# Kernel tuning notes

Hardware: AMD Instinct MI355X
Metric: run time of the kernel (lower is better)

The kernel has to match this reference:

```python
import jax, jax.numpy as jnp
import numpy as np

EPS = 1e-12
IMU_NOISE_DIAG = np.array([1e-07, 1e-07, 0.01, 0.001], dtype=np.float32)
INIT_COVAR_SQRT = np.array([0, 0, 0, 0, 0, 0, 0.01, 0.01, 0.01, 1e-4, 1e-4, 1e-4,
                            1e-08, 1e-08, 1e-08, 0.1, 0.1, 0.1], dtype=np.float32)
TRANS_SCALE = 5.4
TS2 = TRANS_SCALE * TRANS_SCALE
VIS_INIT_GUESS = 10.0 / TS2
VIS_BETA, VIS_GAMMA = 3.0, 1.0
IMU_BETA, IMU_GAMMA = 4.0, 1.0


def skew3(v):  # (..., 3) -> (..., 3, 3)
    x, y, z = v[..., 0], v[..., 1], v[..., 2]
    o = jnp.zeros_like(x)
    return jnp.stack([jnp.stack([o, -z, y], -1),
                      jnp.stack([z, o, -x], -1),
                      jnp.stack([-y, x, o], -1)], -2)


def exp_SO3(phi):  # (..., 3) -> (..., 3, 3) Rodrigues
    theta2 = jnp.sum(phi * phi, axis=-1)
    theta = jnp.sqrt(theta2)
    small = theta < 1e-8
    th = jnp.where(small, 1.0, theta)
    A = jnp.where(small, 1.0 - theta2 / 6.0, jnp.sin(th) / th)[..., None, None]
    B = jnp.where(small, 0.5 - theta2 / 24.0, (1.0 - jnp.cos(th)) / (th * th))[..., None, None]
    K = skew3(phi)
    return jnp.eye(3, dtype=phi.dtype) + A * K + B * (K @ K)


def force_symmetrical(M):
    Mu = jnp.triu(M)
    n = M.shape[-1]
    return Mu + jnp.swapaxes(Mu, -1, -2) * (1.0 - jnp.eye(n, dtype=M.dtype))


def proc_vis_covar(vis_std):
    # vis_covar_scale is all ones (par.vis_covar_scale = 1.0)
    scale = jnp.ones((6,), dtype=vis_std.dtype)
    diag = VIS_INIT_GUESS * (10.0 ** (VIS_BETA * jnp.tanh(VIS_GAMMA * vis_std)))
    diag = diag / scale[None, :]
    return jax.vmap(jnp.diag)(diag)  # (2B, 6, 6)


def get_imu_noise_covar(imu_noise_weight):
    # Linear(1,4,bias=False) applied to ones(1): just the weight column
    covar = 10.0 ** (IMU_BETA * jnp.tanh(IMU_GAMMA * imu_noise_weight[:, 0]))  # (4,)
    diag = jnp.repeat(jnp.asarray(IMU_NOISE_DIAG), 3) * jnp.repeat(covar, 3)   # (12,)
    return jnp.diag(diag)


def propagate(dts, wa_xyzs, R_ckbts, g_k, imu_noise_covar, P0):
    B = dts.shape[0]
    T = dts.shape[1]
    I3 = jnp.eye(3, dtype=dts.dtype)
    I18 = jnp.eye(18, dtype=dts.dtype)

    def step(P, inp):
        dt, gyro, accel, R = inp  # (B,), (B,3), (B,3), (B,3,3)
        Rt = jnp.swapaxes(R, -1, -2)
        w = gyro  # bw_k = 0
        Rg = jnp.einsum('bij,bj->bi', Rt, g_k)
        a = accel - Rg  # ba_k = 0
        F = jnp.zeros((B, 18, 18), dtype=dt.dtype)
        F = F.at[:, 0:3, 0:3].set(-skew3(w))
        F = F.at[:, 0:3, 12:15].set(-I3)
        F = F.at[:, 3:6, 6:9].set(I3)
        F = F.at[:, 6:9, 0:3].set(-jnp.einsum('bij,bjk->bik', R, skew3(Rg + a)))
        F = F.at[:, 6:9, 9:12].set(-I3)
        F = F.at[:, 6:9, 15:18].set(-R)
        G = jnp.zeros((B, 18, 12), dtype=dt.dtype)
        G = G.at[:, 0:3, 0:3].set(-I3)
        G = G.at[:, 6:9, 6:9].set(-R)
        G = G.at[:, 12:15, 3:6].set(I3)
        G = G.at[:, 15:18, 9:12].set(I3)
        dtb = dt[:, None, None]
        Phi = I18 + F * dtb + 0.5 * (F @ F) * (dtb * dtb)
        Phi = Phi.at[:, 0:3, 0:3].set(jnp.swapaxes(exp_SO3(dt[:, None] * w), -1, -2))
        PhiT = jnp.swapaxes(Phi, -1, -2)
        Q = (Phi @ G @ imu_noise_covar @ jnp.swapaxes(G, -1, -2) @ PhiT) * dtb
        P = force_symmetrical(Phi @ P @ PhiT + Q)
        return P, None

    xs = (jnp.swapaxes(dts, 0, 1),                       # (T, B)
          jnp.swapaxes(wa_xyzs[:, :T, :3], 0, 1),        # (T, B, 3)
          jnp.swapaxes(wa_xyzs[:, :T, 3:], 0, 1),        # (T, B, 3)
          jnp.swapaxes(R_ckbts[:, :T], 0, 1))            # (T, B, 3, 3)
    P, _ = jax.lax.scan(step, P0, xs)
    return P


def update(preimu_rot, preimu_trans, P, vis_rot, vis_trans, vis_covar, H0, H1, v_ck, g_ck):
    B = vis_rot.shape[0]
    residual = jnp.concatenate([vis_rot - preimu_rot, vis_trans - preimu_trans], axis=1)  # (B,6)
    I3 = jnp.eye(3, dtype=vis_rot.dtype)
    H = jnp.zeros((B, 6, 18), dtype=vis_rot.dtype)
    H = H.at[:, 0:3, 0:3].set(H0)
    H = H.at[:, 3:6, 0:3].set(H1)
    H = H.at[:, 3:6, 3:6].set(I3)
    Ht = jnp.swapaxes(H, -1, -2)
    S = H @ P @ Ht + vis_covar                 # (B,6,6)
    K = P @ Ht @ jnp.linalg.inv(S)             # (B,18,6)
    est = K @ residual[..., None]              # (B,18,1)
    phi_e, p_e = est[:, 0:3], est[:, 3:6]
    v_e, g_e = est[:, 6:9], est[:, 9:12]
    ekf_phi = preimu_rot + (H0 @ phi_e)[..., 0]
    ekf_t = preimu_trans + (H1 @ phi_e)[..., 0] + p_e[..., 0]
    return ekf_phi, ekf_t, v_ck + v_e[..., 0], g_ck + g_e[..., 0]


def setup_inputs() -> dict:
    key = jax.random.key(0)
    ks = jax.random.split(key, 16)
    B2 = 8192
    d = {
        'dts': jax.random.uniform(ks[0], (B2, 11), jnp.float32) * 0.01,
        'wa_xyzs': jax.random.normal(ks[1], (B2, 12, 6), jnp.float32),
        'R_ckbts': jax.random.normal(ks[2], (B2, 12, 3, 3), jnp.float32),
        'velocities': jax.random.normal(ks[3], (B2, 3), jnp.float32),
        'gravities': jax.random.normal(ks[4], (B2, 3), jnp.float32),
        'H0': jax.random.normal(ks[5], (B2, 3, 3), jnp.float32),
        'H1': jax.random.normal(ks[6], (B2, 3, 3), jnp.float32),
        'preimu_rot': jax.random.normal(ks[7], (B2, 3), jnp.float32),
        'preimu_trans': jax.random.normal(ks[8], (B2, 3), jnp.float32),
        'vis_rot': jax.random.normal(ks[9], (B2, 3), jnp.float32),
        'vis_trans': jax.random.normal(ks[10], (B2, 3), jnp.float32),
        'vis_rot_std': jax.random.uniform(ks[11], (B2, 3), jnp.float32),
        'vis_trans_std': jax.random.uniform(ks[12], (B2, 3), jnp.float32),
        'init_covar_diag_sqrt': jnp.asarray(INIT_COVAR_SQRT),
        'imu_noise_weight': jnp.zeros((4, 1), jnp.float32),  # train_imu_noise_covar=False -> zeroed
    }
    return d


def reference(dts, wa_xyzs, R_ckbts, velocities, gravities, H0, H1,
              preimu_rot, preimu_trans, vis_rot, vis_trans,
              vis_rot_std, vis_trans_std, init_covar_diag_sqrt, imu_noise_weight):
    B2 = dts.shape[0]
    vis_std = jnp.concatenate([vis_rot_std, vis_trans_std], axis=1)
    vis_covar = proc_vis_covar(vis_std)
    vis_trans = vis_trans * TRANS_SCALE
    imu_noise_covar = get_imu_noise_covar(imu_noise_weight)
    P0_diag = init_covar_diag_sqrt * init_covar_diag_sqrt + EPS
    P0 = jnp.broadcast_to(jnp.diag(P0_diag), (B2, 18, 18))
    P = propagate(dts, wa_xyzs, R_ckbts, gravities, imu_noise_covar, P0)
    ekf_phi, ekf_t, ekf_v, ekf_g = update(preimu_rot, preimu_trans, P,
                                          vis_rot, vis_trans, vis_covar,
                                          H0, H1, velocities, gravities)
    return jnp.concatenate([ekf_phi, ekf_t, ekf_v, ekf_g], axis=1)  # (2B, 12)
```

## Files before the change

### kernel.cpp

```cpp
#include <hip/hip_runtime.h>
#include <math.h>

#define TSTEPS 11
#define PPB 7
#define LPP 9
#define IN_STRIDE 196
#define WSTRIDE 228
#define PHT_OFF 0
#define S6_OFF 144
#define Y_OFF 192
#define EST_OFF 200

__device__ __forceinline__ float sel3(int c, float a, float b, float d) {
    float t = (c == 1) ? b : a;
    return (c == 2) ? d : t;
}

__device__ __forceinline__ size_t umin_sz(size_t a, size_t b) { return a < b ? a : b; }

__global__ void __launch_bounds__(64)
ekf_kernel(const float* __restrict__ dts, const float* __restrict__ wa,
           const float* __restrict__ Rc, const float* __restrict__ vel,
           const float* __restrict__ grav, const float* __restrict__ H0g,
           const float* __restrict__ H1g, const float* __restrict__ prot,
           const float* __restrict__ ptrans, const float* __restrict__ vrot,
           const float* __restrict__ vtrans, const float* __restrict__ vrstd,
           const float* __restrict__ vtstd, const float* __restrict__ icds,
           const float* __restrict__ inw, float* __restrict__ out, int B)
{
    __shared__ __align__(16) float gin[PPB * IN_STRIDE];
    __shared__ __align__(16) float lds[PPB * WSTRIDE];
    const int tid = threadIdx.x;
    const int praw = tid / LPP;
    const int r = tid - praw * LPP;
    const int p = (praw < PPB) ? praw : (PPB - 1);
    const int blk0 = blockIdx.x * PPB;
    const int b0 = blk0 + p;
    const bool valid = (praw < PPB) && (b0 < B);
    const int b = (b0 < B) ? b0 : (B - 1);
    float* L = lds + p * WSTRIDE;
    const float* gi = gin + p * IN_STRIDE;

    {
        const size_t dmax = (size_t)B * 11 - 1;
        for (int e = tid; e < PPB * 11; e += 64) {
            const int pp = e / 11, o = e - pp * 11;
            gin[pp * IN_STRIDE + o] = dts[umin_sz((size_t)blk0 * 11 + e, dmax)];
        }
        const size_t wmax4 = (size_t)B * 18 - 1;
        const float4* wa4 = (const float4*)wa;
        for (int e = tid; e < PPB * 18; e += 64) {
            const int pp = e / 18, o = e - pp * 18;
            *(float4*)&gin[pp * IN_STRIDE + 12 + o * 4] = wa4[umin_sz((size_t)blk0 * 18 + e, wmax4)];
        }
        const size_t rmax4 = (size_t)B * 27 - 1;
        const float4* Rc4 = (const float4*)Rc;
        for (int e = tid; e < PPB * 27; e += 64) {
            const int pp = e / 27, o = e - pp * 27;
            *(float4*)&gin[pp * IN_STRIDE + 84 + o * 4] = Rc4[umin_sz((size_t)blk0 * 27 + e, rmax4)];
        }
    }

    float h0v[9], h1v[9];
#pragma unroll
    for (int i = 0; i < 9; ++i) { h0v[i] = H0g[(size_t)b * 9 + i]; h1v[i] = H1g[(size_t)b * 9 + i]; }
    const int rc6 = (r < 6) ? r : 5;
    const float* hpr = (rc6 < 3) ? (H0g + (size_t)b * 9 + rc6 * 3)
                                 : (H1g + (size_t)b * 9 + (rc6 - 3) * 3);
    const float hr0 = hpr[0], hr1 = hpr[1], hr2 = hpr[2];
    const float sdv = (rc6 < 3) ? vrstd[(size_t)b * 3 + rc6] : vtstd[(size_t)b * 3 + (rc6 - 3)];
    const float rsa = (rc6 < 3) ? vrot[(size_t)b * 3 + rc6] : vtrans[(size_t)b * 3 + (rc6 - 3)];
    const float rsb = (rc6 < 3) ? prot[(size_t)b * 3 + rc6] : ptrans[(size_t)b * 3 + (rc6 - 3)];
    const float velv = vel[(size_t)b * 3 + ((r >= 6) ? (r - 6) : 0)];

    const float qcA = 1e-7f * exp10f(4.f * tanhf(inw[0]));
    const float qcB = 1e-7f * exp10f(4.f * tanhf(inw[1]));
    const float qcC = 1e-2f * exp10f(4.f * tanhf(inw[2]));
    const float qcD = 1e-3f * exp10f(4.f * tanhf(inw[3]));

    const float g0 = grav[(size_t)b*3+0], g1 = grav[(size_t)b*3+1], g2 = grav[(size_t)b*3+2];

    float np[18], npb[18];
#pragma unroll
    for (int k = 0; k < 18; ++k) { np[k] = 0.f; npb[k] = 0.f; }
    { const float d0 = icds[r];     np[r]      = d0*d0 + 1e-12f;
      const float d1 = icds[9 + r]; npb[9 + r] = d1*d1 + 1e-12f; }

    __syncthreads();

    for (int t = 0; t < TSTEPS; ++t) {
        const float dt = gi[t];
        const float2 wq0 = *(const float2*)&gi[12 + t * 6];
        const float2 wq1 = *(const float2*)&gi[12 + t * 6 + 2];
        const float2 wq2 = *(const float2*)&gi[12 + t * 6 + 4];
        const float w0 = wq0.x, w1 = wq0.y, w2 = wq1.x;
        const float ar0 = wq1.y, ar1 = wq2.x, ar2 = wq2.y;
        float Rm[9];
#pragma unroll
        for (int i = 0; i < 9; ++i) Rm[i] = gi[84 + t * 9 + i];

        const float hdt2 = 0.5f * dt * dt;
        const float Rg0 = Rm[0]*g0 + Rm[3]*g1 + Rm[6]*g2;
        const float Rg1 = Rm[1]*g0 + Rm[4]*g1 + Rm[7]*g2;
        const float Rg2 = Rm[2]*g0 + Rm[5]*g1 + Rm[8]*g2;
        const float a0 = Rg0 + (ar0 - Rg0);
        const float a1 = Rg1 + (ar1 - Rg1);
        const float a2 = Rg2 + (ar2 - Rg2);

        const float p0 = dt*w0, p1 = dt*w1, p2 = dt*w2;
        const float th2 = p0*p0 + p1*p1 + p2*p2;
        const float th4 = th2 * th2;
        const float A  = 1.f - th2*(1.f/6.f)  + th4*(1.f/120.f);
        const float Bc = 0.5f - th2*(1.f/24.f) + th4*(1.f/720.f);
        float E[9];
        E[0] =  Bc*(p0*p0 - th2);  E[1] =  A*p2 + Bc*p0*p1;  E[2] = -A*p1 + Bc*p0*p2;
        E[3] = -A*p2 + Bc*p1*p0;   E[4] =  Bc*(p1*p1 - th2); E[5] =  A*p0 + Bc*p1*p2;
        E[6] =  A*p1 + Bc*p2*p0;   E[7] = -A*p0 + Bc*p2*p1;  E[8] =  Bc*(p2*p2 - th2);
        float N[9];
        N[0] = -(Rm[1]*a2 - Rm[2]*a1);  N[1] = -(Rm[2]*a0 - Rm[0]*a2);  N[2] = -(Rm[0]*a1 - Rm[1]*a0);
        N[3] = -(Rm[4]*a2 - Rm[5]*a1);  N[4] = -(Rm[5]*a0 - Rm[3]*a2);  N[5] = -(Rm[3]*a1 - Rm[4]*a0);
        N[6] = -(Rm[7]*a2 - Rm[8]*a1);  N[7] = -(Rm[8]*a0 - Rm[6]*a2);  N[8] = -(Rm[6]*a1 - Rm[7]*a0);
        float M2[9];
#pragma unroll
        for (int c = 0; c < 3; ++c) {
            const float n0 = N[c*3], n1 = N[c*3+1], n2 = N[c*3+2];
            M2[c*3+0] = dt*n0 - hdt2*(n1*w2 - n2*w1);
            M2[c*3+1] = dt*n1 - hdt2*(n2*w0 - n0*w2);
            M2[c*3+2] = dt*n2 - hdt2*(n0*w1 - n1*w0);
        }

        auto Smv = [&](const float v[18], float o[9]) {
            const float ev0 = E[0]*v[0] + E[1]*v[1] + E[2]*v[2];
            const float ev1 = E[3]*v[0] + E[4]*v[1] + E[5]*v[2];
            const float ev2 = E[6]*v[0] + E[7]*v[1] + E[8]*v[2];
            const float cx0 = w1*v[14] - w2*v[13];
            const float cx1 = w2*v[12] - w0*v[14];
            const float cx2 = w0*v[13] - w1*v[12];
            o[0] = ev0 - dt*v[12] + hdt2*cx0;
            o[1] = ev1 - dt*v[13] + hdt2*cx1;
            o[2] = ev2 - dt*v[14] + hdt2*cx2;
            const float nv0 = N[0]*v[0] + N[1]*v[1] + N[2]*v[2];
            const float nv1 = N[3]*v[0] + N[4]*v[1] + N[5]*v[2];
            const float nv2 = N[6]*v[0] + N[7]*v[1] + N[8]*v[2];
            const float rv0 = Rm[0]*v[15] + Rm[1]*v[16] + Rm[2]*v[17];
            const float rv1 = Rm[3]*v[15] + Rm[4]*v[16] + Rm[5]*v[17];
            const float rv2 = Rm[6]*v[15] + Rm[7]*v[16] + Rm[8]*v[17];
            o[3] = hdt2*nv0 + dt*v[6] - hdt2*v[9]  - hdt2*rv0;
            o[4] = hdt2*nv1 + dt*v[7] - hdt2*v[10] - hdt2*rv1;
            o[5] = hdt2*nv2 + dt*v[8] - hdt2*v[11] - hdt2*rv2;
            const float mv0 = M2[0]*v[0] + M2[1]*v[1] + M2[2]*v[2];
            const float mv1 = M2[3]*v[0] + M2[4]*v[1] + M2[5]*v[2];
            const float mv2 = M2[6]*v[0] + M2[7]*v[1] + M2[8]*v[2];
            const float nw0 = N[0]*v[12] + N[1]*v[13] + N[2]*v[14];
            const float nw1 = N[3]*v[12] + N[4]*v[13] + N[5]*v[14];
            const float nw2 = N[6]*v[12] + N[7]*v[13] + N[8]*v[14];
            o[6] = mv0 - dt*v[9]  - hdt2*nw0 - dt*rv0;
            o[7] = mv1 - dt*v[10] - hdt2*nw1 - dt*rv1;
            o[8] = mv2 - dt*v[11] - hdt2*nw2 - dt*rv2;
        };

        float uca[9], ucb[9];
        Smv(np, uca);
        Smv(npb, ucb);
#pragma unroll
        for (int i = 0; i < 9; ++i) {
            L[i*20 + r]     = uca[i];
            L[i*20 + 9 + r] = ucb[i];
        }
        __syncthreads();

        float ur[18];
        {
            const float4* up = (const float4*)&L[r*20];
            const float4 q0 = up[0], q1 = up[1], q2 = up[2], q3 = up[3];
            const float2 q4 = *(const float2*)&L[r*20 + 16];
            ur[0]=q0.x; ur[1]=q0.y; ur[2]=q0.z; ur[3]=q0.w;
            ur[4]=q1.x; ur[5]=q1.y; ur[6]=q1.z; ur[7]=q1.w;
            ur[8]=q2.x; ur[9]=q2.y; ur[10]=q2.z; ur[11]=q2.w;
            ur[12]=q3.x; ur[13]=q3.y; ur[14]=q3.z; ur[15]=q3.w;
            ur[16]=q4.x; ur[17]=q4.y;
        }

        float w9[9];
        Smv(ur, w9);

        const int c6 = (r >= 6) ? (r - 6) : 0;
        const float rc0 = sel3(c6, Rm[0], Rm[3], Rm[6]);
        const float rc1 = sel3(c6, Rm[1], Rm[4], Rm[7]);
        const float rc2 = sel3(c6, Rm[2], Rm[5], Rm[8]);
        const float dq = dt * qcC;
        const float q0v = dq * (Rm[0]*rc0 + Rm[1]*rc1 + Rm[2]*rc2);
        const float q1v = dq * (Rm[3]*rc0 + Rm[4]*rc1 + Rm[5]*rc2);
        const float q2v = dq * (Rm[6]*rc0 + Rm[7]*rc1 + Rm[8]*rc2);

#pragma unroll
        for (int i = 0; i < 9; ++i)
            np[i] = np[i] + uca[i] + ur[i] + w9[i];
        if (r < 3) np[r] += dt * qcA;
        if (r >= 6) { np[6] += q0v; np[7] += q1v; np[8] += q2v; }
#pragma unroll
        for (int i = 9; i < 18; ++i) np[i] += ur[i];

#pragma unroll
        for (int i = 0; i < 9; ++i) npb[i] += ucb[i];
        if (r >= 3) npb[9 + r] += dt * ((r < 6) ? qcB : qcD);

        __syncthreads();
    }

    float phtA[6], phtB[6];
#pragma unroll
    for (int m = 0; m < 3; ++m) {
        phtA[m] = np[0]*h0v[m*3] + np[1]*h0v[m*3+1] + np[2]*h0v[m*3+2];
        phtB[m] = npb[0]*h0v[m*3] + npb[1]*h0v[m*3+1] + npb[2]*h0v[m*3+2];
    }
#pragma unroll
    for (int m = 3; m < 6; ++m) {
        phtA[m] = np[0]*h1v[(m-3)*3] + np[1]*h1v[(m-3)*3+1] + np[2]*h1v[(m-3)*3+2] + np[m];
        phtB[m] = npb[0]*h1v[(m-3)*3] + npb[1]*h1v[(m-3)*3+1] + npb[2]*h1v[(m-3)*3+2] + npb[m];
    }
#pragma unroll
    for (int m = 0; m < 6; ++m) {
        L[PHT_OFF + r*8 + m]       = phtA[m];
        L[PHT_OFF + (9 + r)*8 + m] = phtB[m];
    }
    __syncthreads();

    if (valid && r < 6) {
        const float VIG = (float)(10.0 / (5.4 * 5.4));
#pragma unroll
        for (int n = 0; n < 6; ++n) {
            float v = hr0 * L[PHT_OFF + 0*8 + n] + hr1 * L[PHT_OFF + 1*8 + n]
                    + hr2 * L[PHT_OFF + 2*8 + n];
            if (r >= 3) v += phtA[n];
            if (n == r) v += VIG * exp10f(3.f * tanhf(sdv));
            L[S6_OFF + r*8 + n] = v;
        }
        L[S6_OFF + r*8 + 6] = (r < 3) ? (rsa - rsb) : (rsa * 5.4f - rsb);
    }
    __syncthreads();

    if (valid && r == 0) {
        float a[6][7];
        const float* Sb = &L[S6_OFF];
#pragma unroll
        for (int m = 0; m < 6; ++m) {
            const float4 q0 = *(const float4*)&Sb[m*8];
            const float4 q1 = *(const float4*)&Sb[m*8 + 4];
            a[m][0]=q0.x; a[m][1]=q0.y; a[m][2]=q0.z; a[m][3]=q0.w;
            a[m][4]=q1.x; a[m][5]=q1.y; a[m][6]=q1.z;
        }
#pragma unroll
        for (int k = 0; k < 6; ++k) {
#pragma unroll
            for (int j = k + 1; j < 6; ++j) {
                const bool c = fabsf(a[j][k]) > fabsf(a[k][k]);
#pragma unroll
                for (int cc = k; cc < 7; ++cc) {
                    const float hi = c ? a[j][cc] : a[k][cc];
                    const float lo = c ? a[k][cc] : a[j][cc];
                    a[k][cc] = hi; a[j][cc] = lo;
                }
            }
            const float inv = 1.f / a[k][k];
#pragma unroll
            for (int j = 0; j < 6; ++j) {
                if (j == k) continue;
                const float f = a[j][k] * inv;
#pragma unroll
                for (int cc = k + 1; cc < 7; ++cc) a[j][cc] -= f * a[k][cc];
            }
        }
#pragma unroll
        for (int m = 0; m < 6; ++m) L[Y_OFF + m] = a[m][6] / a[m][m];
    }
    __syncthreads();

    float ym[6];
#pragma unroll
    for (int m = 0; m < 6; ++m) ym[m] = L[Y_OFF + m];
    float estr = 0.f, est9 = 0.f;
#pragma unroll
    for (int m = 0; m < 6; ++m) { estr += phtA[m]*ym[m]; est9 += phtB[m]*ym[m]; }
    if (valid) {
        L[EST_OFF + r] = estr;
        if (r < 3) L[EST_OFF + 9 + r] = est9;
    }
    __syncthreads();

    const float e0 = L[EST_OFF + 0], e1 = L[EST_OFF + 1], e2 = L[EST_OFF + 2];
    if (valid) {
        float o;
        if (r < 3) {
            o = rsb + hr0*e0 + hr1*e1 + hr2*e2;
        } else if (r < 6) {
            o = rsb + hr0*e0 + hr1*e1 + hr2*e2 + estr;
        } else {
            o = velv + estr;
        }
        out[(size_t)b*12 + r] = o;
        if (r < 3) out[(size_t)b*12 + 9 + r] = ((r==0)?g0:((r==1)?g1:g2)) + est9;
    }
}

extern "C" void kernel_launch(void* const* d_in, const int* in_sizes, int n_in,
                              void* d_out, int out_size, void* d_ws, size_t ws_size,
                              hipStream_t stream) {
    const float* dts    = (const float*)d_in[0];
    const float* wa     = (const float*)d_in[1];
    const float* Rc     = (const float*)d_in[2];
    const float* vel    = (const float*)d_in[3];
    const float* grav   = (const float*)d_in[4];
    const float* H0g    = (const float*)d_in[5];
    const float* H1g    = (const float*)d_in[6];
    const float* prot   = (const float*)d_in[7];
    const float* ptrans = (const float*)d_in[8];
    const float* vrot   = (const float*)d_in[9];
    const float* vtrans = (const float*)d_in[10];
    const float* vrstd  = (const float*)d_in[11];
    const float* vtstd  = (const float*)d_in[12];
    const float* icds   = (const float*)d_in[13];
    const float* inw    = (const float*)d_in[14];
    float* outp = (float*)d_out;

    const int B = in_sizes[0] / TSTEPS;
    const int grid = (B + PPB - 1) / PPB;
    hipLaunchKernelGGL(ekf_kernel, dim3(grid), dim3(64), 0, stream,
                       dts, wa, Rc, vel, grav, H0g, H1g, prot, ptrans,
                       vrot, vtrans, vrstd, vtstd, icds, inw, outp, B);
}
```

Measured before the change: 33.73 us.

## Exploit sparse bottom-right covariance block and prefetch next step inputs

Each lane now holds only the lower-right diagonal entry and the off-diagonal cross terms of the covariance block. The bottom-block matrix-vector product is replaced by a closed-form sparse update that uses per-lane column selects of R, N and the gyro skew matrix. Shared-memory input is repacked into a per-timestep record with a stride of 20, and the next step's inputs are read during the current step so LDS latency overlaps compute. The change relies on the bottom-right block staying diagonal, and it adds select logic plus scalar rather than vector global loads during staging.

```diff
diff --git a/kernel.cpp b/kernel.cpp
--- a/kernel.cpp
+++ b/kernel.cpp
@@ -4,7 +4,7 @@
 #define TSTEPS 11
 #define PPB 7
 #define LPP 9
-#define IN_STRIDE 196
+#define IN_STRIDE 228
 #define WSTRIDE 228
 #define PHT_OFF 0
 #define S6_OFF 144
@@ -45,19 +45,21 @@
         const size_t dmax = (size_t)B * 11 - 1;
         for (int e = tid; e < PPB * 11; e += 64) {
             const int pp = e / 11, o = e - pp * 11;
-            gin[pp * IN_STRIDE + o] = dts[umin_sz((size_t)blk0 * 11 + e, dmax)];
-        }
-        const size_t wmax4 = (size_t)B * 18 - 1;
-        const float4* wa4 = (const float4*)wa;
-        for (int e = tid; e < PPB * 18; e += 64) {
-            const int pp = e / 18, o = e - pp * 18;
-            *(float4*)&gin[pp * IN_STRIDE + 12 + o * 4] = wa4[umin_sz((size_t)blk0 * 18 + e, wmax4)];
-        }
-        const size_t rmax4 = (size_t)B * 27 - 1;
-        const float4* Rc4 = (const float4*)Rc;
-        for (int e = tid; e < PPB * 27; e += 64) {
-            const int pp = e / 27, o = e - pp * 27;
-            *(float4*)&gin[pp * IN_STRIDE + 84 + o * 4] = Rc4[umin_sz((size_t)blk0 * 27 + e, rmax4)];
+            gin[pp * IN_STRIDE + o * 20] = dts[umin_sz((size_t)blk0 * 11 + e, dmax)];
+        }
+        const size_t wmax = (size_t)B * 72 - 1;
+        for (int e = tid; e < PPB * 66; e += 64) {
+            const int pp = e / 66, o = e - pp * 66;
+            const int t = o / 6, k = o - t * 6;
+            gin[pp * IN_STRIDE + t * 20 + 2 + k] =
+                wa[umin_sz((size_t)blk0 * 72 + (size_t)pp * 72 + o, wmax)];
+        }
+        const size_t rmax = (size_t)B * 108 - 1;
+        for (int e = tid; e < PPB * 99; e += 64) {
+            const int pp = e / 99, o = e - pp * 99;
+            const int t = o / 9, k = o - t * 9;
+            gin[pp * IN_STRIDE + t * 20 + 8 + k] =
+                Rc[umin_sz((size_t)blk0 * 108 + (size_t)pp * 108 + o, rmax)];
         }
     }
 
@@ -80,24 +82,43 @@
 
     const float g0 = grav[(size_t)b*3+0], g1 = grav[(size_t)b*3+1], g2 = grav[(size_t)b*3+2];
 
-    float np[18], npb[18];
-#pragma unroll
-    for (int k = 0; k < 18; ++k) { np[k] = 0.f; npb[k] = 0.f; }
-    { const float d0 = icds[r];     np[r]      = d0*d0 + 1e-12f;
-      const float d1 = icds[9 + r]; npb[9 + r] = d1*d1 + 1e-12f; }
-
-    __syncthreads();
+    float np[18], ncr[9];
+#pragma unroll
+    for (int k = 0; k < 18; ++k) np[k] = 0.f;
+#pragma unroll
+    for (int k = 0; k < 9; ++k) ncr[k] = 0.f;
+    float d_br;
+    { const float d0 = icds[r];     np[r] = d0*d0 + 1e-12f;
+      const float d1 = icds[9 + r]; d_br  = d1*d1 + 1e-12f; }
+
+    const int cls = (r < 3) ? 0 : ((r < 6) ? 1 : 2);
+    const int c3 = r - 3 * cls;
+
+    __syncthreads();
+
+    float dt = gi[0];
+    float w0, w1, w2, ar0, ar1, ar2, Rm[9];
+    {
+        const float2 qa = *(const float2*)&gi[2];
+        const float2 qb = *(const float2*)&gi[4];
+        const float2 qc = *(const float2*)&gi[6];
+        w0 = qa.x; w1 = qa.y; w2 = qb.x; ar0 = qb.y; ar1 = qc.x; ar2 = qc.y;
+        const float4 r0 = *(const float4*)&gi[8];
+        const float4 r1 = *(const float4*)&gi[12];
+        Rm[0]=r0.x; Rm[1]=r0.y; Rm[2]=r0.z; Rm[3]=r0.w;
+        Rm[4]=r1.x; Rm[5]=r1.y; Rm[6]=r1.z; Rm[7]=r1.w;
+        Rm[8]=gi[16];
+    }
 
     for (int t = 0; t < TSTEPS; ++t) {
-        const float dt = gi[t];
-        const float2 wq0 = *(const float2*)&gi[12 + t * 6];
-        const float2 wq1 = *(const float2*)&gi[12 + t * 6 + 2];
-        const float2 wq2 = *(const float2*)&gi[12 + t * 6 + 4];
-        const float w0 = wq0.x, w1 = wq0.y, w2 = wq1.x;
-        const float ar0 = wq1.y, ar1 = wq2.x, ar2 = wq2.y;
-        float Rm[9];
-#pragma unroll
-        for (int i = 0; i < 9; ++i) Rm[i] = gi[84 + t * 9 + i];
+        const int tn = (t + 1 < TSTEPS) ? (t + 1) : t;
+        const float dt_n = gi[tn*20];
+        const float2 nqa = *(const float2*)&gi[tn*20 + 2];
+        const float2 nqb = *(const float2*)&gi[tn*20 + 4];
+        const float2 nqc = *(const float2*)&gi[tn*20 + 6];
+        const float4 nr0 = *(const float4*)&gi[tn*20 + 8];
+        const float4 nr1 = *(const float4*)&gi[tn*20 + 12];
+        const float nr8 = gi[tn*20 + 16];
 
         const float hdt2 = 0.5f * dt * dt;
         const float Rg0 = Rm[0]*g0 + Rm[3]*g1 + Rm[6]*g2;
@@ -159,9 +180,46 @@
             o[8] = mv2 - dt*v[11] - hdt2*nw2 - dt*rv2;
         };
 
-        float uca[9], ucb[9];
+        float uca[9];
         Smv(np, uca);
-        Smv(npb, ucb);
+
+        float ucb[9];
+        {
+            const float colR0 = sel3(c3, Rm[0], Rm[1], Rm[2]);
+            const float colR1 = sel3(c3, Rm[3], Rm[4], Rm[5]);
+            const float colR2 = sel3(c3, Rm[6], Rm[7], Rm[8]);
+            const float colN0 = sel3(c3, N[0], N[1], N[2]);
+            const float colN1 = sel3(c3, N[3], N[4], N[5]);
+            const float colN2 = sel3(c3, N[6], N[7], N[8]);
+            const float colK0 = sel3(c3, 0.f, -w2,  w1);
+            const float colK1 = sel3(c3,  w2, 0.f, -w0);
+            const float colK2 = sel3(c3, -w1,  w0, 0.f);
+            const float e0c = (c3 == 0) ? 1.f : 0.f;
+            const float e1c = (c3 == 1) ? 1.f : 0.f;
+            const float e2c = (c3 == 2) ? 1.f : 0.f;
+            const float dbdt = d_br * dt, dbh = d_br * hdt2;
+
+            const float s00 = (cls == 1) ? (-dbdt*e0c + dbh*colK0) : 0.f;
+            const float s01 = (cls == 1) ? (-dbdt*e1c + dbh*colK1) : 0.f;
+            const float s02 = (cls == 1) ? (-dbdt*e2c + dbh*colK2) : 0.f;
+            const float s30 = (cls == 0) ? -dbh*e0c : ((cls == 2) ? -dbh*colR0 : 0.f);
+            const float s31 = (cls == 0) ? -dbh*e1c : ((cls == 2) ? -dbh*colR1 : 0.f);
+            const float s32 = (cls == 0) ? -dbh*e2c : ((cls == 2) ? -dbh*colR2 : 0.f);
+            const float s60 = (cls == 0) ? -dbdt*e0c : ((cls == 1) ? -dbh*colN0 : -dbdt*colR0);
+            const float s61 = (cls == 0) ? -dbdt*e1c : ((cls == 1) ? -dbh*colN1 : -dbdt*colR1);
+            const float s62 = (cls == 0) ? -dbdt*e2c : ((cls == 1) ? -dbh*colN2 : -dbdt*colR2);
+
+            ucb[0] = E[0]*ncr[0] + E[1]*ncr[1] + E[2]*ncr[2] + s00;
+            ucb[1] = E[3]*ncr[0] + E[4]*ncr[1] + E[5]*ncr[2] + s01;
+            ucb[2] = E[6]*ncr[0] + E[7]*ncr[1] + E[8]*ncr[2] + s02;
+            ucb[3] = hdt2*(N[0]*ncr[0] + N[1]*ncr[1] + N[2]*ncr[2]) + dt*ncr[6] + s30;
+            ucb[4] = hdt2*(N[3]*ncr[0] + N[4]*ncr[1] + N[5]*ncr[2]) + dt*ncr[7] + s31;
+            ucb[5] = hdt2*(N[6]*ncr[0] + N[7]*ncr[1] + N[8]*ncr[2]) + dt*ncr[8] + s32;
+            ucb[6] = M2[0]*ncr[0] + M2[1]*ncr[1] + M2[2]*ncr[2] + s60;
+            ucb[7] = M2[3]*ncr[0] + M2[4]*ncr[1] + M2[5]*ncr[2] + s61;
+            ucb[8] = M2[6]*ncr[0] + M2[7]*ncr[1] + M2[8]*ncr[2] + s62;
+        }
+
 #pragma unroll
         for (int i = 0; i < 9; ++i) {
             L[i*20 + r]     = uca[i];
@@ -181,18 +239,17 @@
             ur[16]=q4.x; ur[17]=q4.y;
         }
 
-        float w9[9];
-        Smv(ur, w9);
-
-        const int c6 = (r >= 6) ? (r - 6) : 0;
-        const float rc0 = sel3(c6, Rm[0], Rm[3], Rm[6]);
-        const float rc1 = sel3(c6, Rm[1], Rm[4], Rm[7]);
-        const float rc2 = sel3(c6, Rm[2], Rm[5], Rm[8]);
+        const float rc0 = sel3(c3, Rm[0], Rm[3], Rm[6]);
+        const float rc1 = sel3(c3, Rm[1], Rm[4], Rm[7]);
+        const float rc2 = sel3(c3, Rm[2], Rm[5], Rm[8]);
         const float dq = dt * qcC;
         const float q0v = dq * (Rm[0]*rc0 + Rm[1]*rc1 + Rm[2]*rc2);
         const float q1v = dq * (Rm[3]*rc0 + Rm[4]*rc1 + Rm[5]*rc2);
         const float q2v = dq * (Rm[6]*rc0 + Rm[7]*rc1 + Rm[8]*rc2);
 
+        float w9[9];
+        Smv(ur, w9);
+
 #pragma unroll
         for (int i = 0; i < 9; ++i)
             np[i] = np[i] + uca[i] + ur[i] + w9[i];
@@ -202,22 +259,28 @@
         for (int i = 9; i < 18; ++i) np[i] += ur[i];
 
 #pragma unroll
-        for (int i = 0; i < 9; ++i) npb[i] += ucb[i];
-        if (r >= 3) npb[9 + r] += dt * ((r < 6) ? qcB : qcD);
+        for (int i = 0; i < 9; ++i) ncr[i] += ucb[i];
+        if (r >= 3) d_br += dt * ((r < 6) ? qcB : qcD);
 
         __syncthreads();
+
+        dt = dt_n;
+        w0 = nqa.x; w1 = nqa.y; w2 = nqb.x; ar0 = nqb.y; ar1 = nqc.x; ar2 = nqc.y;
+        Rm[0]=nr0.x; Rm[1]=nr0.y; Rm[2]=nr0.z; Rm[3]=nr0.w;
+        Rm[4]=nr1.x; Rm[5]=nr1.y; Rm[6]=nr1.z; Rm[7]=nr1.w;
+        Rm[8]=nr8;
     }
 
     float phtA[6], phtB[6];
 #pragma unroll
     for (int m = 0; m < 3; ++m) {
         phtA[m] = np[0]*h0v[m*3] + np[1]*h0v[m*3+1] + np[2]*h0v[m*3+2];
-        phtB[m] = npb[0]*h0v[m*3] + npb[1]*h0v[m*3+1] + npb[2]*h0v[m*3+2];
+        phtB[m] = ncr[0]*h0v[m*3] + ncr[1]*h0v[m*3+1] + ncr[2]*h0v[m*3+2];
     }
 #pragma unroll
     for (int m = 3; m < 6; ++m) {
         phtA[m] = np[0]*h1v[(m-3)*3] + np[1]*h1v[(m-3)*3+1] + np[2]*h1v[(m-3)*3+2] + np[m];
-        phtB[m] = npb[0]*h1v[(m-3)*3] + npb[1]*h1v[(m-3)*3+1] + npb[2]*h1v[(m-3)*3+2] + npb[m];
+        phtB[m] = ncr[0]*h1v[(m-3)*3] + ncr[1]*h1v[(m-3)*3+1] + ncr[2]*h1v[(m-3)*3+2] + ncr[m];
     }
 #pragma unroll
     for (int m = 0; m < 6; ++m) {
```

After: 34.50 us. 2.3% more time.
